# Performance work log

Hardware: AMD Instinct MI355X
Metric: run time of the kernel (lower is better)

Reference implementation:

```python
import jax, jax.numpy as jnp
import numpy as np

B, S, IN, OUT = 4, 2048, 4096, 16384

def setup_inputs() -> dict:
    key = jax.random.key(0)
    k1, k2, k3, k4 = jax.random.split(key, 4)
    x = jax.random.normal(k1, (B, S, IN), dtype=jnp.float32)
    quantized_weight = jax.random.randint(k2, (OUT, IN), 0, 16, dtype=jnp.int32)
    scale = jax.random.uniform(k3, (OUT,), dtype=jnp.float32)
    zero_point = jax.random.randint(k4, (OUT,), 0, 16, dtype=jnp.int32)
    return {"x": x, "quantized_weight": quantized_weight, "scale": scale, "zero_point": zero_point}

def reference(x, quantized_weight, scale, zero_point):
    # Per-output-channel dequantization: W = (q - zp) * scale, shape [OUT, IN]
    weight = (quantized_weight.astype(jnp.float32) - zero_point.astype(jnp.float32)[:, None]) * scale[:, None]
    # F.linear(x, W) = x @ W.T -> [B, S, OUT]
    return jnp.einsum('bsi,oi->bso', x, weight)
```

## Files before the change

### kernel.cpp

```cpp
#include <hip/hip_runtime.h>
#include <stdint.h>

#define MDIM 8192
#define NDIM 16384
#define KDIM 4096
#define NT   64
#define PSTR 1048576

typedef __attribute__((ext_vector_type(4)))  int i32x4;
typedef __attribute__((ext_vector_type(16))) int i32x16;

__device__ __forceinline__ void gload_lds16(const void* g, void* l) {
    __builtin_amdgcn_global_load_lds(
        (const __attribute__((address_space(1))) void*)g,
        (__attribute__((address_space(3))) void*)l,
        16, 0, 0);
}

__device__ __forceinline__ i32x16 MFMA32(i32x4 a, i32x4 b, i32x16 c) {
    return __builtin_amdgcn_mfma_i32_32x32x32_i8(a, b, c, 0, 0, 0);
}


__global__ __launch_bounds__(256)
void rowmax_kernel(const float* __restrict__ x, float* __restrict__ sx,
                   float* __restrict__ invx) {
    const int row = (int)blockIdx.x;
    const float4* xr = (const float4*)(x + (long)row * KDIM);
    const int t = threadIdx.x;
    float m = 0.f;
#pragma unroll
    for (int i = 0; i < 4; ++i) {
        float4 v = xr[t + 256 * i];
        m = fmaxf(m, fmaxf(fmaxf(fabsf(v.x), fabsf(v.y)), fmaxf(fabsf(v.z), fabsf(v.w))));
    }
#pragma unroll
    for (int off = 32; off >= 1; off >>= 1) m = fmaxf(m, __shfl_xor(m, off));
    __shared__ float red[4];
    if ((t & 63) == 0) red[t >> 6] = m;
    __syncthreads();
    m = fmaxf(fmaxf(red[0], red[1]), fmaxf(red[2], red[3]));
    m = fmaxf(m, 1e-20f);
    if (t == 0) { sx[row] = m * (1.0f / 127.0f); invx[row] = 127.0f / m; }
}

__global__ __launch_bounds__(256)
void quantx_t_kernel(const float* __restrict__ x, const float* __restrict__ invx,
                     int8_t* __restrict__ xq) {
    const int b  = (int)blockIdx.x;
    const int p  = b >> 8, tt = (b >> 2) & 63, c = b & 3;
    const int pr = threadIdx.x;
    const long row = (long)p * 256 + pr;
    const float inv = invx[row];
    const float4* src = (const float4*)(x + row * KDIM + tt * 64 + c * 16);
    union { int8_t ch[16]; int4 v; } r;
#pragma unroll
    for (int j = 0; j < 4; ++j) {
        float4 v = src[j];
        r.ch[j * 4 + 0] = (int8_t)__float2int_rn(v.x * inv);
        r.ch[j * 4 + 1] = (int8_t)__float2int_rn(v.y * inv);
        r.ch[j * 4 + 2] = (int8_t)__float2int_rn(v.z * inv);
        r.ch[j * 4 + 3] = (int8_t)__float2int_rn(v.w * inv);
    }
    *(int4*)(xq + (long)p * PSTR + tt * 16384 + c * 4096 + pr * 16) = r.v;
}

__global__ __launch_bounds__(256)
void quantw_t_kernel(const int* __restrict__ q, const int* __restrict__ zp,
                     int8_t* __restrict__ wq) {
    const int b  = (int)blockIdx.x;
    const int p  = b >> 8, tt = (b >> 2) & 63, c = b & 3;
    const int pr = threadIdx.x;
    const long o = (long)p * 256 + pr;
    const int z = zp[o];
    const int4* src = (const int4*)(q + o * KDIM + tt * 64 + c * 16);
    union { int8_t ch[16]; int4 v; } r;
#pragma unroll
    for (int j = 0; j < 4; ++j) {
        int4 a = src[j];
        r.ch[j * 4 + 0] = (int8_t)(a.x - z);
        r.ch[j * 4 + 1] = (int8_t)(a.y - z);
        r.ch[j * 4 + 2] = (int8_t)(a.z - z);
        r.ch[j * 4 + 3] = (int8_t)(a.w - z);
    }
    *(int4*)(wq + (long)p * PSTR + tt * 16384 + c * 4096 + pr * 16) = r.v;
}


__global__ __launch_bounds__(512, 2)
void gemm_i8_kernel(const int8_t* __restrict__ A, const int8_t* __restrict__ Wt,
                    const float* __restrict__ scale, const float* __restrict__ sx,
                    float* __restrict__ C) {
    __shared__ int8_t lds[3 * 32768];

    const int wg = (int)blockIdx.x;
    const int rr = wg >> 8;
    const int ii = wg & 255;
    const int bm = ii & 31;
    const int bn = rr * 8 + (ii >> 5);

    const int tid  = threadIdx.x;
    const int lane = tid & 63;
    const int wid  = tid >> 6;
    const int wm   = wid >> 2;
    const int wn   = wid & 3;
    const int l31  = lane & 31;
    const int lh   = lane >> 5;

    const int dl = tid * 16;

    const int8_t* Ab = A  + (long)bm * PSTR;
    const int8_t* Wb = Wt + (long)bn * PSTR;

#define STAGE(bb, P, base, tt)                                                      \
    do {                                                                            \
        gload_lds16((base) + (tt) * 16384 + dl,        &lds[(bb) + (P) * 16384 + dl]);        \
        gload_lds16((base) + (tt) * 16384 + 8192 + dl, &lds[(bb) + (P) * 16384 + 8192 + dl]); \
    } while (0)

#define RDA2(DST, BB, MTB)                                                          \
    _Pragma("unroll")                                                               \
    for (int m_ = 0; m_ < 2; ++m_)                                                  \
        _Pragma("unroll")                                                           \
        for (int k_ = 0; k_ < 2; ++k_)                                              \
            DST[m_ * 2 + k_] = *(const i32x4*)&lds[(BB) + ((k_ * 2 + lh) << 12) +   \
                ((wm * 128 + ((MTB) + m_) * 32 + l31) << 4)];

#define RDB(DST, BB)                                                                \
    _Pragma("unroll")                                                               \
    for (int n_ = 0; n_ < 2; ++n_)                                                  \
        _Pragma("unroll")                                                           \
        for (int k_ = 0; k_ < 2; ++k_)                                              \
            DST[n_ * 2 + k_] = *(const i32x4*)&lds[(BB) + 16384 +                   \
                ((k_ * 2 + lh) << 12) + ((wn * 64 + n_ * 32 + l31) << 4)];

#define MFH(MB, AS, BS)                                                             \
    do {                                                                            \
        __builtin_amdgcn_sched_barrier(0);                                          \
        __builtin_amdgcn_s_setprio(1);                                              \
        _Pragma("unroll")                                                           \
        for (int m_ = 0; m_ < 2; ++m_)                                              \
            _Pragma("unroll")                                                       \
            for (int n_ = 0; n_ < 2; ++n_)                                          \
                _Pragma("unroll")                                                   \
                for (int k_ = 0; k_ < 2; ++k_)                                      \
                    acc[(MB) + m_][n_] = MFMA32(AS[m_ * 2 + k_], BS[n_ * 2 + k_],   \
                                                acc[(MB) + m_][n_]);                \
        __builtin_amdgcn_s_setprio(0);                                              \
        __builtin_amdgcn_sched_barrier(0);                                          \
    } while (0)

    i32x16 acc[4][2];
#pragma unroll
    for (int i = 0; i < 4; ++i)
#pragma unroll
        for (int j = 0; j < 2; ++j)
#pragma unroll
            for (int r = 0; r < 16; ++r) acc[i][j][r] = 0;

    i32x4 aS0[4], aHi[4], bSA[4], bSB[4];
    int b0 = 0, b1 = 32768, b2 = 65536;

    STAGE(b0, 0, Ab, 0); STAGE(b0, 1, Wb, 0);
    STAGE(b1, 0, Ab, 1); STAGE(b1, 1, Wb, 1);
    asm volatile("s_waitcnt vmcnt(4)" ::: "memory");
    __builtin_amdgcn_s_barrier();
    RDA2(aS0, b0, 0);
    RDB(bSA, b0);

#define KSTEP(T, BCUR, BNXT)                                                        \
    do {                                                                            \
        const bool pf_ = (T) < NT - 2;                                              \
                   \
        RDA2(aHi, b0, 2);                                                           \
        if (pf_) { STAGE(b2, 0, Ab, (T) + 2); }                                     \
        MFH(0, aS0, BCUR);                                                          \
               \
        asm volatile("s_waitcnt lgkmcnt(0)" ::: "memory");                          \
        if (pf_) asm volatile("s_waitcnt vmcnt(2)" ::: "memory");                   \
        else     asm volatile("s_waitcnt vmcnt(0)" ::: "memory");                   \
        __builtin_amdgcn_s_barrier();                                               \
        RDA2(aS0, b1, 0);                                                           \
        RDB(BNXT, b1);                                                              \
        if (pf_) { STAGE(b2, 1, Wb, (T) + 2); }                                     \
        MFH(2, aHi, BCUR);                                                          \
        const int tb_ = b0; b0 = b1; b1 = b2; b2 = tb_;                             \
    } while (0)

    for (int t = 0; t < NT; t += 2) {
        KSTEP(t,     bSA, bSB);
        KSTEP(t + 1, bSB, bSA);
    }
#undef KSTEP
#undef STAGE
#undef RDA2
#undef RDB
#undef MFH

    const long rowA0 = (long)bm * 256 + wm * 128;
    const int  colB0 = bn * 256 + wn * 64;
    float scj[2];
#pragma unroll
    for (int n = 0; n < 2; ++n) scj[n] = scale[colB0 + n * 32 + l31];
#pragma unroll
    for (int mt = 0; mt < 4; ++mt) {
#pragma unroll
        for (int g = 0; g < 4; ++g) {
            const long rb = rowA0 + mt * 32 + g * 8 + lh * 4;
            const float4 s4 = *(const float4*)(sx + rb);
#pragma unroll
            for (int n = 0; n < 2; ++n) {
                float* cp = C + rb * NDIM + colB0 + n * 32 + l31;
                cp[0 * (long)NDIM] = (float)acc[mt][n][g * 4 + 0] * scj[n] * s4.x;
                cp[1 * (long)NDIM] = (float)acc[mt][n][g * 4 + 1] * scj[n] * s4.y;
                cp[2 * (long)NDIM] = (float)acc[mt][n][g * 4 + 2] * scj[n] * s4.z;
                cp[3 * (long)NDIM] = (float)acc[mt][n][g * 4 + 3] * scj[n] * s4.w;
            }
        }
    }
}


__global__ __launch_bounds__(256)
void fallback_kernel(const float* __restrict__ x, const int* __restrict__ q,
                     const float* __restrict__ scale, const int* __restrict__ zp,
                     float* __restrict__ out) {
    __shared__ float sA[64][17];
    __shared__ float sB[64][17];
    const int bn = (int)blockIdx.x % (NDIM / 64);
    const int bm = (int)blockIdx.x / (NDIM / 64);
    const int t  = threadIdx.x;
    const int tx = t & 15, ty = t >> 4;
    const long rowA = (long)bm * 64, rowB = (long)bn * 64;
    float acc[4][4] = {};
    for (int k0 = 0; k0 < KDIM; k0 += 16) {
#pragma unroll
        for (int i = 0; i < 4; ++i) {
            const int e = t + i * 256;
            const int r = e >> 4, c = e & 15;
            sA[r][c] = x[(rowA + r) * KDIM + k0 + c];
            const int o = (int)rowB + r;
            sB[r][c] = (float)(q[(long)o * KDIM + k0 + c] - zp[o]) * scale[o];
        }
        __syncthreads();
#pragma unroll
        for (int kk = 0; kk < 16; ++kk) {
            float a[4], b[4];
#pragma unroll
            for (int i = 0; i < 4; ++i) a[i] = sA[ty * 4 + i][kk];
#pragma unroll
            for (int j = 0; j < 4; ++j) b[j] = sB[tx * 4 + j][kk];
#pragma unroll
            for (int i = 0; i < 4; ++i)
#pragma unroll
                for (int j = 0; j < 4; ++j) acc[i][j] += a[i] * b[j];
        }
        __syncthreads();
    }
#pragma unroll
    for (int i = 0; i < 4; ++i) {
        const long r = rowA + ty * 4 + i;
#pragma unroll
        for (int j = 0; j < 4; ++j)
            out[r * NDIM + rowB + tx * 4 + j] = acc[i][j];
    }
}


extern "C" void kernel_launch(void* const* d_in, const int* in_sizes, int n_in,
                              void* d_out, int out_size, void* d_ws, size_t ws_size,
                              hipStream_t stream) {
    const float* x     = (const float*)d_in[0];
    const int*   qw    = (const int*)d_in[1];
    const float* scale = (const float*)d_in[2];
    const int*   zp    = (const int*)d_in[3];
    float*       out   = (float*)d_out;

    const size_t needA  = (size_t)MDIM * KDIM;
    const size_t needW  = (size_t)NDIM * KDIM;
    const size_t needSx = (size_t)MDIM * sizeof(float);
    const size_t needIx = (size_t)MDIM * sizeof(float);

    if (ws_size >= needA + needW + needSx + needIx) {
        int8_t* xq = (int8_t*)d_ws;
        int8_t* wq = xq + needA;
        float*  sx = (float*)((char*)d_ws + needA + needW);
        float*  ix = sx + MDIM;
        rowmax_kernel<<<MDIM, 256, 0, stream>>>(x, sx, ix);
        quantx_t_kernel<<<(MDIM / 256) * 64 * 4, 256, 0, stream>>>(x, ix, xq);
        quantw_t_kernel<<<(NDIM / 256) * 64 * 4, 256, 0, stream>>>(qw, zp, wq);
        gemm_i8_kernel<<<(MDIM / 256) * (NDIM / 256), 512, 0, stream>>>(xq, wq, scale, sx, out);
    } else {
        fallback_kernel<<<(MDIM / 64) * (NDIM / 64), 256, 0, stream>>>(x, qw, scale, zp, out);
    }
}
```

Baseline: 775.5 us.

## Shrink GEMM tile to 128x128 with double buffering and LDS-staged quant transposes

```diff
diff --git a/kernel.cpp b/kernel.cpp
--- a/kernel.cpp
+++ b/kernel.cpp
@@ -45,165 +45,163 @@
 }
 
 __global__ __launch_bounds__(256)
-void quantx_t_kernel(const float* __restrict__ x, const float* __restrict__ invx,
-                     int8_t* __restrict__ xq) {
-    const int b  = (int)blockIdx.x;
-    const int p  = b >> 8, tt = (b >> 2) & 63, c = b & 3;
-    const int pr = threadIdx.x;
-    const long row = (long)p * 256 + pr;
-    const float inv = invx[row];
-    const float4* src = (const float4*)(x + row * KDIM + tt * 64 + c * 16);
-    union { int8_t ch[16]; int4 v; } r;
-#pragma unroll
-    for (int j = 0; j < 4; ++j) {
-        float4 v = src[j];
-        r.ch[j * 4 + 0] = (int8_t)__float2int_rn(v.x * inv);
-        r.ch[j * 4 + 1] = (int8_t)__float2int_rn(v.y * inv);
-        r.ch[j * 4 + 2] = (int8_t)__float2int_rn(v.z * inv);
-        r.ch[j * 4 + 3] = (int8_t)__float2int_rn(v.w * inv);
-    }
-    *(int4*)(xq + (long)p * PSTR + tt * 16384 + c * 4096 + pr * 16) = r.v;
-}
-
-__global__ __launch_bounds__(256)
-void quantw_t_kernel(const int* __restrict__ q, const int* __restrict__ zp,
-                     int8_t* __restrict__ wq) {
-    const int b  = (int)blockIdx.x;
-    const int p  = b >> 8, tt = (b >> 2) & 63, c = b & 3;
-    const int pr = threadIdx.x;
-    const long o = (long)p * 256 + pr;
-    const int z = zp[o];
-    const int4* src = (const int4*)(q + o * KDIM + tt * 64 + c * 16);
-    union { int8_t ch[16]; int4 v; } r;
-#pragma unroll
-    for (int j = 0; j < 4; ++j) {
-        int4 a = src[j];
-        r.ch[j * 4 + 0] = (int8_t)(a.x - z);
-        r.ch[j * 4 + 1] = (int8_t)(a.y - z);
-        r.ch[j * 4 + 2] = (int8_t)(a.z - z);
-        r.ch[j * 4 + 3] = (int8_t)(a.w - z);
-    }
-    *(int4*)(wq + (long)p * PSTR + tt * 16384 + c * 4096 + pr * 16) = r.v;
-}
-
-
-__global__ __launch_bounds__(512, 2)
+void quantx_t2(const float* __restrict__ x, const float* __restrict__ invx,
+               int8_t* __restrict__ xq) {
+    __shared__ int4 tb[1024];
+    const int b = (int)blockIdx.x;
+    const int p = b >> 6, tt = b & 63;
+    const int tid = threadIdx.x;
+#pragma unroll
+    for (int i = 0; i < 4; ++i) {
+        const int idx = i * 256 + tid;
+        const int row = idx >> 2, c = idx & 3;
+        const float inv = invx[p * 256 + row];
+        const float4* src = (const float4*)(x + ((long)p * 256 + row) * KDIM + tt * 64 + c * 16);
+        union { int8_t ch[16]; int4 v; } r;
+#pragma unroll
+        for (int j = 0; j < 4; ++j) {
+            float4 v = src[j];
+            r.ch[j * 4 + 0] = (int8_t)__float2int_rn(v.x * inv);
+            r.ch[j * 4 + 1] = (int8_t)__float2int_rn(v.y * inv);
+            r.ch[j * 4 + 2] = (int8_t)__float2int_rn(v.z * inv);
+            r.ch[j * 4 + 3] = (int8_t)__float2int_rn(v.w * inv);
+        }
+        tb[c * 256 + row] = r.v;
+    }
+    __syncthreads();
+    int4* dst = (int4*)(xq + (long)p * PSTR + (long)tt * 16384);
+#pragma unroll
+    for (int i = 0; i < 4; ++i) {
+        const int idx = i * 256 + tid;
+        dst[idx] = tb[idx];
+    }
+}
+
+__global__ __launch_bounds__(256)
+void quantw_t2(const int* __restrict__ q, const int* __restrict__ zp,
+               int8_t* __restrict__ wq) {
+    __shared__ int4 tb[1024];
+    const int b = (int)blockIdx.x;
+    const int p = b >> 6, tt = b & 63;
+    const int tid = threadIdx.x;
+#pragma unroll
+    for (int i = 0; i < 4; ++i) {
+        const int idx = i * 256 + tid;
+        const int row = idx >> 2, c = idx & 3;
+        const int z = zp[p * 256 + row];
+        const int4* src = (const int4*)(q + ((long)p * 256 + row) * KDIM + tt * 64 + c * 16);
+        union { int8_t ch[16]; int4 v; } r;
+#pragma unroll
+        for (int j = 0; j < 4; ++j) {
+            int4 a = src[j];
+            r.ch[j * 4 + 0] = (int8_t)(a.x - z);
+            r.ch[j * 4 + 1] = (int8_t)(a.y - z);
+            r.ch[j * 4 + 2] = (int8_t)(a.z - z);
+            r.ch[j * 4 + 3] = (int8_t)(a.w - z);
+        }
+        tb[c * 256 + row] = r.v;
+    }
+    __syncthreads();
+    int4* dst = (int4*)(wq + (long)p * PSTR + (long)tt * 16384);
+#pragma unroll
+    for (int i = 0; i < 4; ++i) {
+        const int idx = i * 256 + tid;
+        dst[idx] = tb[idx];
+    }
+}
+
+
+__global__ __launch_bounds__(256, 2)
 void gemm_i8_kernel(const int8_t* __restrict__ A, const int8_t* __restrict__ Wt,
                     const float* __restrict__ scale, const float* __restrict__ sx,
                     float* __restrict__ C) {
-    __shared__ int8_t lds[3 * 32768];
-
-    const int wg = (int)blockIdx.x;
-    const int rr = wg >> 8;
-    const int ii = wg & 255;
-    const int bm = ii & 31;
-    const int bn = rr * 8 + (ii >> 5);
+    __shared__ int8_t lds[2][16384];
+
+    const int wg  = (int)blockIdx.x;
+    const int rr  = wg >> 9;
+    const int ii  = wg & 511;
+    const int bm2 = ii & 63;
+    const int bn2 = rr * 8 + (ii >> 6);
 
     const int tid  = threadIdx.x;
     const int lane = tid & 63;
     const int wid  = tid >> 6;
-    const int wm   = wid >> 2;
-    const int wn   = wid & 3;
+    const int wm   = wid >> 1;
+    const int wn   = wid & 1;
     const int l31  = lane & 31;
     const int lh   = lane >> 5;
 
-    const int dl = tid * 16;
-
-    const int8_t* Ab = A  + (long)bm * PSTR;
-    const int8_t* Wb = Wt + (long)bn * PSTR;
-
-#define STAGE(bb, P, base, tt)                                                      \
+    const int fA = lh * 2048 + (wm * 64 + l31) * 16;
+    const int fB = 8192 + lh * 2048 + (wn * 64 + l31) * 16;
+
+    const int s0 = tid, s1 = tid + 256;
+    const int g0 = (s0 >> 7) * 4096 + (s0 & 127) * 16;
+    const int g1 = (s1 >> 7) * 4096 + (s1 & 127) * 16;
+
+    const int8_t* pA = A  + (long)(bm2 >> 1) * PSTR + (bm2 & 1) * 2048;
+    const int8_t* pB = Wt + (long)(bn2 >> 1) * PSTR + (bn2 & 1) * 2048;
+
+#define STAGE(BUF, TT)                                                              \
     do {                                                                            \
-        gload_lds16((base) + (tt) * 16384 + dl,        &lds[(bb) + (P) * 16384 + dl]);        \
-        gload_lds16((base) + (tt) * 16384 + 8192 + dl, &lds[(bb) + (P) * 16384 + 8192 + dl]); \
+        const int ko_ = (TT) * 16384;                                               \
+        gload_lds16(pA + ko_ + g0, &lds[BUF][s0 * 16]);                             \
+        gload_lds16(pA + ko_ + g1, &lds[BUF][s1 * 16]);                             \
+        gload_lds16(pB + ko_ + g0, &lds[BUF][8192 + s0 * 16]);                      \
+        gload_lds16(pB + ko_ + g1, &lds[BUF][8192 + s1 * 16]);                      \
     } while (0)
 
-#define RDA2(DST, BB, MTB)                                                          \
-    _Pragma("unroll")                                                               \
-    for (int m_ = 0; m_ < 2; ++m_)                                                  \
-        _Pragma("unroll")                                                           \
-        for (int k_ = 0; k_ < 2; ++k_)                                              \
-            DST[m_ * 2 + k_] = *(const i32x4*)&lds[(BB) + ((k_ * 2 + lh) << 12) +   \
-                ((wm * 128 + ((MTB) + m_) * 32 + l31) << 4)];
-
-#define RDB(DST, BB)                                                                \
-    _Pragma("unroll")                                                               \
-    for (int n_ = 0; n_ < 2; ++n_)                                                  \
-        _Pragma("unroll")                                                           \
-        for (int k_ = 0; k_ < 2; ++k_)                                              \
-            DST[n_ * 2 + k_] = *(const i32x4*)&lds[(BB) + 16384 +                   \
-                ((k_ * 2 + lh) << 12) + ((wn * 64 + n_ * 32 + l31) << 4)];
-
-#define MFH(MB, AS, BS)                                                             \
-    do {                                                                            \
-        __builtin_amdgcn_sched_barrier(0);                                          \
-        __builtin_amdgcn_s_setprio(1);                                              \
-        _Pragma("unroll")                                                           \
-        for (int m_ = 0; m_ < 2; ++m_)                                              \
-            _Pragma("unroll")                                                       \
-            for (int n_ = 0; n_ < 2; ++n_)                                          \
-                _Pragma("unroll")                                                   \
-                for (int k_ = 0; k_ < 2; ++k_)                                      \
-                    acc[(MB) + m_][n_] = MFMA32(AS[m_ * 2 + k_], BS[n_ * 2 + k_],   \
-                                                acc[(MB) + m_][n_]);                \
-        __builtin_amdgcn_s_setprio(0);                                              \
-        __builtin_amdgcn_sched_barrier(0);                                          \
-    } while (0)
-
-    i32x16 acc[4][2];
-#pragma unroll
-    for (int i = 0; i < 4; ++i)
+    i32x16 acc[2][2];
+#pragma unroll
+    for (int i = 0; i < 2; ++i)
 #pragma unroll
         for (int j = 0; j < 2; ++j)
 #pragma unroll
             for (int r = 0; r < 16; ++r) acc[i][j][r] = 0;
 
-    i32x4 aS0[4], aHi[4], bSA[4], bSB[4];
-    int b0 = 0, b1 = 32768, b2 = 65536;
-
-    STAGE(b0, 0, Ab, 0); STAGE(b0, 1, Wb, 0);
-    STAGE(b1, 0, Ab, 1); STAGE(b1, 1, Wb, 1);
-    asm volatile("s_waitcnt vmcnt(4)" ::: "memory");
+    STAGE(0, 0);
+    asm volatile("s_waitcnt vmcnt(0)" ::: "memory");
     __builtin_amdgcn_s_barrier();
-    RDA2(aS0, b0, 0);
-    RDB(bSA, b0);
-
-#define KSTEP(T, BCUR, BNXT)                                                        \
-    do {                                                                            \
-        const bool pf_ = (T) < NT - 2;                                              \
-                   \
-        RDA2(aHi, b0, 2);                                                           \
-        if (pf_) { STAGE(b2, 0, Ab, (T) + 2); }                                     \
-        MFH(0, aS0, BCUR);                                                          \
-               \
-        asm volatile("s_waitcnt lgkmcnt(0)" ::: "memory");                          \
-        if (pf_) asm volatile("s_waitcnt vmcnt(2)" ::: "memory");                   \
-        else     asm volatile("s_waitcnt vmcnt(0)" ::: "memory");                   \
-        __builtin_amdgcn_s_barrier();                                               \
-        RDA2(aS0, b1, 0);                                                           \
-        RDB(BNXT, b1);                                                              \
-        if (pf_) { STAGE(b2, 1, Wb, (T) + 2); }                                     \
-        MFH(2, aHi, BCUR);                                                          \
-        const int tb_ = b0; b0 = b1; b1 = b2; b2 = tb_;                             \
-    } while (0)
-
-    for (int t = 0; t < NT; t += 2) {
-        KSTEP(t,     bSA, bSB);
-        KSTEP(t + 1, bSB, bSA);
-    }
-#undef KSTEP
+
+    for (int t = 0; t < NT; ++t) {
+        const int cur = t & 1;
+        const bool pf = (t + 1 < NT);
+        if (pf) STAGE(cur ^ 1, t + 1);
+
+        i32x4 aF[4], bF[4];
+#pragma unroll
+        for (int mt = 0; mt < 2; ++mt)
+#pragma unroll
+            for (int ks = 0; ks < 2; ++ks)
+                aF[mt * 2 + ks] = *(const i32x4*)&lds[cur][fA + ks * 4096 + mt * 512];
+#pragma unroll
+        for (int nt = 0; nt < 2; ++nt)
+#pragma unroll
+            for (int ks = 0; ks < 2; ++ks)
+                bF[nt * 2 + ks] = *(const i32x4*)&lds[cur][fB + ks * 4096 + nt * 512];
+
+        __builtin_amdgcn_s_setprio(1);
+#pragma unroll
+        for (int mt = 0; mt < 2; ++mt)
+#pragma unroll
+            for (int nt = 0; nt < 2; ++nt)
+#pragma unroll
+                for (int ks = 0; ks < 2; ++ks)
+                    acc[mt][nt] = MFMA32(aF[mt * 2 + ks], bF[nt * 2 + ks], acc[mt][nt]);
+        __builtin_amdgcn_s_setprio(0);
+
+        asm volatile("s_waitcnt lgkmcnt(0)" ::: "memory");
+        if (pf) asm volatile("s_waitcnt vmcnt(0)" ::: "memory");
+        __builtin_amdgcn_s_barrier();
+    }
 #undef STAGE
-#undef RDA2
-#undef RDB
-#undef MFH
-
-    const long rowA0 = (long)bm * 256 + wm * 128;
-    const int  colB0 = bn * 256 + wn * 64;
+
+    const long rowA0 = (long)bm2 * 128 + wm * 64;
+    const int  colB0 = bn2 * 128 + wn * 64;
     float scj[2];
 #pragma unroll
     for (int n = 0; n < 2; ++n) scj[n] = scale[colB0 + n * 32 + l31];
 #pragma unroll
-    for (int mt = 0; mt < 4; ++mt) {
+    for (int mt = 0; mt < 2; ++mt) {
 #pragma unroll
         for (int g = 0; g < 4; ++g) {
             const long rb = rowA0 + mt * 32 + g * 8 + lh * 4;
@@ -287,9 +285,9 @@
         float*  sx = (float*)((char*)d_ws + needA + needW);
         float*  ix = sx + MDIM;
         rowmax_kernel<<<MDIM, 256, 0, stream>>>(x, sx, ix);
-        quantx_t_kernel<<<(MDIM / 256) * 64 * 4, 256, 0, stream>>>(x, ix, xq);
-        quantw_t_kernel<<<(NDIM / 256) * 64 * 4, 256, 0, stream>>>(qw, zp, wq);
-        gemm_i8_kernel<<<(MDIM / 256) * (NDIM / 256), 512, 0, stream>>>(xq, wq, scale, sx, out);
+        quantx_t2<<<(MDIM / 256) * 64, 256, 0, stream>>>(x, ix, xq);
+        quantw_t2<<<(NDIM / 256) * 64, 256, 0, stream>>>(qw, zp, wq);
+        gemm_i8_kernel<<<(MDIM / 128) * (NDIM / 128), 256, 0, stream>>>(xq, wq, scale, sx, out);
     } else {
         fallback_kernel<<<(MDIM / 64) * (NDIM / 64), 256, 0, stream>>>(x, qw, scale, zp, out);
     }
```

Result: slower. 811.7 us (+4.7%).
